# Kernel optimization log

Hardware: AMD Instinct MI355X
Metric: run time of the kernel (lower is better)

The kernel has to match this reference:

```python
import jax, jax.numpy as jnp
import numpy as np

SEQ, B, I, H = 2048, 64, 512, 512


def setup_inputs() -> dict:
    key = jax.random.key(0)
    ks = jax.random.split(key, 5)
    s = 1.0 / np.sqrt(H)  # torch.nn.RNN init scale
    return {
        "x": jax.random.normal(ks[0], (SEQ, B, I), dtype=jnp.float32),
        "W_ih": jax.random.normal(ks[1], (H, I), dtype=jnp.float32) * s,
        "W_hh": jax.random.normal(ks[2], (H, H), dtype=jnp.float32) * s,
        "b_ih": jax.random.normal(ks[3], (H,), dtype=jnp.float32) * s,
        "b_hh": jax.random.normal(ks[4], (H,), dtype=jnp.float32) * s,
    }


def reference(x, W_ih, W_hh, b_ih, b_hh):
    # Precompute input projection for all timesteps in one big GEMM: [T,B,H]
    xw = jnp.einsum("tbi,hi->tbh", x, W_ih) + b_ih + b_hh

    def step(h, xt):
        # h: [B,H]; xt: [B,H] (already includes x_t W_ih^T + biases)
        h = jnp.tanh(xt + h @ W_hh.T)
        return h, h

    h0 = jnp.zeros((x.shape[1], W_hh.shape[0]), dtype=x.dtype)
    _, out = jax.lax.scan(step, h0, xw)  # out: [T,B,H]
    return out.reshape(-1, W_hh.shape[0])  # [T*B, H], matches out.view(-1, hidden)
```

## Files before the change

### kernel.cpp

```cpp
#include <hip/hip_runtime.h>
#include <cmath>


#define SEQ_T 2048
#define BATCH 64
#define KDIM 512
#define HDIM 512

typedef __fp16 h2v __attribute__((ext_vector_type(2)));
typedef __fp16 f16x8 __attribute__((ext_vector_type(8)));
typedef float f32x4 __attribute__((ext_vector_type(4)));

static __device__ __forceinline__ f16x8 pk8(float4 a, float4 b) {
  h2v p0 = __builtin_amdgcn_cvt_pkrtz(a.x, a.y);
  h2v p1 = __builtin_amdgcn_cvt_pkrtz(a.z, a.w);
  h2v p2 = __builtin_amdgcn_cvt_pkrtz(b.x, b.y);
  h2v p3 = __builtin_amdgcn_cvt_pkrtz(b.z, b.w);
  f16x8 r;
  r[0] = p0[0]; r[1] = p0[1]; r[2] = p1[0]; r[3] = p1[1];
  r[4] = p2[0]; r[5] = p2[1]; r[6] = p3[0]; r[7] = p3[1];
  return r;
}


#define G_LDA 72

#define MFM(mt, nt) \
  d##mt##nt = __builtin_amdgcn_mfma_f32_16x16x32_f16(fa##mt, fb##nt, d##mt##nt, 0, 0, 0);

#define EPI(mt, nt, bb)                                                     \
  {                                                                         \
    int row = m0 + wm + mt * 16 + (l >> 4) * 4;                             \
    int col = n0 + wn + nt * 16 + (l & 15);                                 \
    out[(size_t)(row + 0) * HDIM + col] = d##mt##nt[0] + bb;                \
    out[(size_t)(row + 1) * HDIM + col] = d##mt##nt[1] + bb;                \
    out[(size_t)(row + 2) * HDIM + col] = d##mt##nt[2] + bb;                \
    out[(size_t)(row + 3) * HDIM + col] = d##mt##nt[3] + bb;                \
  }

__global__ __launch_bounds__(256) void xw_gemm(const float* __restrict__ x,
                                               const float* __restrict__ Wih,
                                               const float* __restrict__ bih,
                                               const float* __restrict__ bhh,
                                               float* __restrict__ out) {
  __shared__ __fp16 At[128 * G_LDA];
  __shared__ __fp16 Bt[64 * G_LDA];
  const int tid = threadIdx.x;
  const int l = tid & 63;
  const int w = tid >> 6;
  const int m0 = (blockIdx.x >> 3) * 128;
  const int n0 = (blockIdx.x & 7) * 64;
  const int wm = (w >> 1) * 64;
  const int wn = (w & 1) * 32;

  const float bias0 = bih[n0 + wn + (l & 15)] + bhh[n0 + wn + (l & 15)];
  const float bias1 = bih[n0 + wn + 16 + (l & 15)] + bhh[n0 + wn + 16 + (l & 15)];

  f32x4 d00 = {0,0,0,0}, d01 = {0,0,0,0}, d10 = {0,0,0,0}, d11 = {0,0,0,0};
  f32x4 d20 = {0,0,0,0}, d21 = {0,0,0,0}, d30 = {0,0,0,0}, d31 = {0,0,0,0};

  for (int k0 = 0; k0 < KDIM; k0 += 64) {
    __syncthreads();
#pragma unroll
    for (int p = 0; p < 4; ++p) {
      int idx = tid + p * 256;
      int r = idx >> 3, sg = idx & 7;
      const float* ps = x + (size_t)(m0 + r) * KDIM + k0 + sg * 8;
      *(f16x8*)(At + r * G_LDA + sg * 8) =
          pk8(*(const float4*)ps, *(const float4*)(ps + 4));
    }
#pragma unroll
    for (int p = 0; p < 2; ++p) {
      int idx = tid + p * 256;
      int r = idx >> 3, sg = idx & 7;
      const float* ps = Wih + (size_t)(n0 + r) * KDIM + k0 + sg * 8;
      *(f16x8*)(Bt + r * G_LDA + sg * 8) =
          pk8(*(const float4*)ps, *(const float4*)(ps + 4));
    }
    __syncthreads();
#pragma unroll
    for (int kk = 0; kk < 2; ++kk) {
      const int kc = kk * 32 + (l >> 4) * 8;
      f16x8 fa0 = *(const f16x8*)(At + (wm + 0 * 16 + (l & 15)) * G_LDA + kc);
      f16x8 fa1 = *(const f16x8*)(At + (wm + 1 * 16 + (l & 15)) * G_LDA + kc);
      f16x8 fa2 = *(const f16x8*)(At + (wm + 2 * 16 + (l & 15)) * G_LDA + kc);
      f16x8 fa3 = *(const f16x8*)(At + (wm + 3 * 16 + (l & 15)) * G_LDA + kc);
      f16x8 fb0 = *(const f16x8*)(Bt + (wn + 0 * 16 + (l & 15)) * G_LDA + kc);
      f16x8 fb1 = *(const f16x8*)(Bt + (wn + 1 * 16 + (l & 15)) * G_LDA + kc);
      MFM(0, 0) MFM(1, 0) MFM(2, 0) MFM(3, 0)
      MFM(0, 1) MFM(1, 1) MFM(2, 1) MFM(3, 1)
    }
  }

  EPI(0, 0, bias0) EPI(1, 0, bias0) EPI(2, 0, bias0) EPI(3, 0, bias0)
  EPI(0, 1, bias1) EPI(1, 1, bias1) EPI(2, 1, bias1) EPI(3, 1, bias1)
}


#define REPB(M, c) M(c,0) M(c,1) M(c,2) M(c,3) M(c,4) M(c,5) \
                   M(c,6) M(c,7) M(c,8) M(c,9) M(c,10) M(c,11)

#define DECLB(c, n) f16x8 bf##c##_##n;
#define LOADB(c, n)                                        \
  {                                                        \
    const float* p = wr##c + 32 * n;                       \
    bf##c##_##n = pk8(*(const float4*)p, *(const float4*)(p + 4)); \
  }
#define STOREB(c, n)                                                        \
  {                                                                         \
    const float* p = wr##c + 32 * n;                                        \
    *(f16x8*)(ldsm + ((n - 12) * 4 + c) * 8192 + (tid << 4)) =              \
        pk8(*(const float4*)p, *(const float4*)(p + 4));                    \
  }

#define MF(c, n) \
  d##c = __builtin_amdgcn_mfma_f32_16x16x32_f16(acur, bf##c##_##n, d##c, 0, 0, 0);
#define MFL(c, n)                                                           \
  {                                                                         \
    f16x8 bl = *(const f16x8*)(ldsm + ((n - 12) * 4 + c) * 8192 + (tid << 4)); \
    d##c = __builtin_amdgcn_mfma_f32_16x16x32_f16(acur, bl, d##c, 0, 0, 0); \
  }

#define CH(n, nn)                                                \
  {                                                              \
    f16x8 anx = *(const f16x8*)(hcv + 64 * (nn) + goff);         \
    MF(0, n) MF(1, n) MF(2, n) MF(3, n)                          \
    acur = anx;                                                  \
  }
#define CHL(n, nn)                                               \
  {                                                              \
    f16x8 anx = *(const f16x8*)(hcv + 64 * (nn) + goff);         \
    MFL(0, n) MFL(1, n) MFL(2, n) MFL(3, n)                      \
    acur = anx;                                                  \
  }

#define WLDS_BYTES (16 * 8192)
#define HBUF0 WLDS_BYTES
#define LDS_TOTAL (WLDS_BYTES + 3 * 1024)

__global__ __attribute__((amdgpu_flat_work_group_size(512, 512),
                          amdgpu_waves_per_eu(2, 2)))
void rnn_scan(const float* __restrict__ Whh, float* __restrict__ io) {
  extern __shared__ __align__(16) char ldsm[];
  const int tid = threadIdx.x;
  const int b = blockIdx.x;
  const int l = tid & 63;
  const int w = tid >> 6;
  const int m16 = l & 15;
  const int gh = l >> 4;
  const int goff = gh << 4;
  const int rb = w << 6;
  const int jo = rb + l;

  const float* wr0 = Whh + (size_t)(rb + 0 + m16) * KDIM + 8 * gh;
  const float* wr1 = Whh + (size_t)(rb + 16 + m16) * KDIM + 8 * gh;
  const float* wr2 = Whh + (size_t)(rb + 32 + m16) * KDIM + 8 * gh;
  const float* wr3 = Whh + (size_t)(rb + 48 + m16) * KDIM + 8 * gh;

  REPB(DECLB, 0) REPB(DECLB, 1) REPB(DECLB, 2) REPB(DECLB, 3)
  REPB(LOADB, 0) REPB(LOADB, 1) REPB(LOADB, 2) REPB(LOADB, 3)

  STOREB(0, 12) STOREB(1, 12) STOREB(2, 12) STOREB(3, 12)
  STOREB(0, 13) STOREB(1, 13) STOREB(2, 13) STOREB(3, 13)
  STOREB(0, 14) STOREB(1, 14) STOREB(2, 14) STOREB(3, 14)
  STOREB(0, 15) STOREB(1, 15) STOREB(2, 15) STOREB(3, 15)

  if (tid < 512) ((unsigned short*)(ldsm + HBUF0))[tid] = 0;
  __syncthreads();

  char* hcur = ldsm + HBUF0;
  char* hnxt = ldsm + HBUF0 + 1024;
  char* hthr = ldsm + HBUF0 + 2048;

  float* iorow = io + (size_t)b * HDIM;

  for (int t = 0; t < SEQ_T; ++t) {
    float uin = iorow[jo];

    const char* hcv = hcur;
    f16x8 acur = *(const f16x8*)(hcv + goff);

    f32x4 d0 = {0.f, 0.f, 0.f, 0.f};
    f32x4 d1 = {0.f, 0.f, 0.f, 0.f};
    f32x4 d2 = {0.f, 0.f, 0.f, 0.f};
    f32x4 d3 = {0.f, 0.f, 0.f, 0.f};

    CH(0, 1)  CH(1, 2)  CH(2, 3)   CH(3, 4)   CH(4, 5)   CH(5, 6)
    CH(6, 7)  CH(7, 8)  CH(8, 9)   CH(9, 10)  CH(10, 11) CH(11, 12)
    CHL(12, 13) CHL(13, 14) CHL(14, 15) CHL(15, 15)

    float za = (l & 16) ? d1[0] : d0[0];
    float zb = (l & 16) ? d3[0] : d2[0];
    float zs = (l & 32) ? zb : za;

    float z = uin + zs;
    float e = __expf(2.0f * z);
    float hn = 1.0f - 2.0f * __builtin_amdgcn_rcpf(e + 1.0f);
    iorow[jo] = hn;
    *(__fp16*)(hnxt + 2 * jo) = (__fp16)hn;

    char* tmp = hcur;
    hcur = hnxt; hnxt = hthr; hthr = tmp;
    iorow += (size_t)BATCH * HDIM;
    __syncthreads();
  }
}

extern "C" void kernel_launch(void* const* d_in, const int* in_sizes, int n_in,
                              void* d_out, int out_size, void* d_ws, size_t ws_size,
                              hipStream_t stream) {
  const float* x = (const float*)d_in[0];
  const float* Wih = (const float*)d_in[1];
  const float* Whh = (const float*)d_in[2];
  const float* bih = (const float*)d_in[3];
  const float* bhh = (const float*)d_in[4];
  float* out = (float*)d_out;

  (void)hipFuncSetAttribute((const void*)rnn_scan,
                            hipFuncAttributeMaxDynamicSharedMemorySize,
                            LDS_TOTAL);

  const int M = SEQ_T * BATCH;
  dim3 g1((M / 128) * (HDIM / 64));
  xw_gemm<<<g1, 256, 0, stream>>>(x, Wih, bih, bhh, out);

  rnn_scan<<<BATCH, 512, LDS_TOTAL, stream>>>(Whh, out);
}
```

Baseline: 3.358 ms.

## Stream half of W_hh fragments from global per step instead of LDS

A new prep kernel packs the upper half of W_hh (k-chunks 8-15) into fp16 MFMA fragment layout in the workspace. The scan kernel keeps only chunks 0-7 in registers and reloads the other half from global memory (L2-resident) every timestep, interleaved with the MFMAs. LDS use drops to the 3 KB hidden-state buffers. This removes the per-step LDS reads of weights and frees registers, but adds global/L2 load latency on the serial critical path of every step.

```diff
diff --git a/kernel.cpp b/kernel.cpp
--- a/kernel.cpp
+++ b/kernel.cpp
@@ -22,6 +22,15 @@
   return r;
 }
 
+__global__ __launch_bounds__(256) void w_prep(const float* __restrict__ Whh,
+                                              f16x8* __restrict__ ws) {
+  int v = blockIdx.x * 256 + threadIdx.x;
+  int l = v & 63, w = (v >> 6) & 7, c = (v >> 9) & 3, n = (v >> 11) + 8;
+  int row = 64 * w + 16 * c + (l & 15);
+  int col = 32 * n + 8 * (l >> 4);
+  const float* p = Whh + (size_t)row * KDIM + col;
+  ws[v] = pk8(*(const float4*)p, *(const float4*)(p + 4));
+}
 
 #define G_LDA 72
 
@@ -97,8 +106,7 @@
 }
 
 
-#define REPB(M, c) M(c,0) M(c,1) M(c,2) M(c,3) M(c,4) M(c,5) \
-                   M(c,6) M(c,7) M(c,8) M(c,9) M(c,10) M(c,11)
+#define REPB(M, c) M(c,0) M(c,1) M(c,2) M(c,3) M(c,4) M(c,5) M(c,6) M(c,7)
 
 #define DECLB(c, n) f16x8 bf##c##_##n;
 #define LOADB(c, n)                                        \
@@ -106,20 +114,18 @@
     const float* p = wr##c + 32 * n;                       \
     bf##c##_##n = pk8(*(const float4*)p, *(const float4*)(p + 4)); \
   }
-#define STOREB(c, n)                                                        \
-  {                                                                         \
-    const float* p = wr##c + 32 * n;                                        \
-    *(f16x8*)(ldsm + ((n - 12) * 4 + c) * 8192 + (tid << 4)) =              \
-        pk8(*(const float4*)p, *(const float4*)(p + 4));                    \
-  }
+
+#define DECLS(n) f16x8 sv0_##n, sv1_##n, sv2_##n, sv3_##n;
+#define LOADS(n)                                  \
+  sv0_##n = wsp[((n - 8) * 4 + 0) * 512];         \
+  sv1_##n = wsp[((n - 8) * 4 + 1) * 512];         \
+  sv2_##n = wsp[((n - 8) * 4 + 2) * 512];         \
+  sv3_##n = wsp[((n - 8) * 4 + 3) * 512];
 
 #define MF(c, n) \
   d##c = __builtin_amdgcn_mfma_f32_16x16x32_f16(acur, bf##c##_##n, d##c, 0, 0, 0);
-#define MFL(c, n)                                                           \
-  {                                                                         \
-    f16x8 bl = *(const f16x8*)(ldsm + ((n - 12) * 4 + c) * 8192 + (tid << 4)); \
-    d##c = __builtin_amdgcn_mfma_f32_16x16x32_f16(acur, bl, d##c, 0, 0, 0); \
-  }
+#define MS(c, n) \
+  d##c = __builtin_amdgcn_mfma_f32_16x16x32_f16(acur, sv##c##_##n, d##c, 0, 0, 0);
 
 #define CH(n, nn)                                                \
   {                                                              \
@@ -127,21 +133,18 @@
     MF(0, n) MF(1, n) MF(2, n) MF(3, n)                          \
     acur = anx;                                                  \
   }
-#define CHL(n, nn)                                               \
+#define CST(n, nn)                                               \
   {                                                              \
     f16x8 anx = *(const f16x8*)(hcv + 64 * (nn) + goff);         \
-    MFL(0, n) MFL(1, n) MFL(2, n) MFL(3, n)                      \
+    MS(0, n) MS(1, n) MS(2, n) MS(3, n)                          \
     acur = anx;                                                  \
   }
-
-#define WLDS_BYTES (16 * 8192)
-#define HBUF0 WLDS_BYTES
-#define LDS_TOTAL (WLDS_BYTES + 3 * 1024)
 
 __global__ __attribute__((amdgpu_flat_work_group_size(512, 512),
                           amdgpu_waves_per_eu(2, 2)))
-void rnn_scan(const float* __restrict__ Whh, float* __restrict__ io) {
-  extern __shared__ __align__(16) char ldsm[];
+void rnn_scan(const float* __restrict__ Whh, const f16x8* __restrict__ ws,
+              float* __restrict__ io) {
+  __shared__ __align__(16) char ldsm[3 * 1024];
   const int tid = threadIdx.x;
   const int b = blockIdx.x;
   const int l = tid & 63;
@@ -160,19 +163,19 @@
   REPB(DECLB, 0) REPB(DECLB, 1) REPB(DECLB, 2) REPB(DECLB, 3)
   REPB(LOADB, 0) REPB(LOADB, 1) REPB(LOADB, 2) REPB(LOADB, 3)
 
-  STOREB(0, 12) STOREB(1, 12) STOREB(2, 12) STOREB(3, 12)
-  STOREB(0, 13) STOREB(1, 13) STOREB(2, 13) STOREB(3, 13)
-  STOREB(0, 14) STOREB(1, 14) STOREB(2, 14) STOREB(3, 14)
-  STOREB(0, 15) STOREB(1, 15) STOREB(2, 15) STOREB(3, 15)
-
-  if (tid < 512) ((unsigned short*)(ldsm + HBUF0))[tid] = 0;
+  const f16x8* wsp = ws + (w * 64 + l);
+
+  if (tid < 512) ((unsigned short*)ldsm)[tid] = 0;
   __syncthreads();
 
-  char* hcur = ldsm + HBUF0;
-  char* hnxt = ldsm + HBUF0 + 1024;
-  char* hthr = ldsm + HBUF0 + 2048;
+  char* hcur = ldsm;
+  char* hnxt = ldsm + 1024;
+  char* hthr = ldsm + 2048;
 
   float* iorow = io + (size_t)b * HDIM;
+
+  DECLS(8) DECLS(9) DECLS(10) DECLS(11)
+  DECLS(12) DECLS(13) DECLS(14) DECLS(15)
 
   for (int t = 0; t < SEQ_T; ++t) {
     float uin = iorow[jo];
@@ -185,9 +188,17 @@
     f32x4 d2 = {0.f, 0.f, 0.f, 0.f};
     f32x4 d3 = {0.f, 0.f, 0.f, 0.f};
 
-    CH(0, 1)  CH(1, 2)  CH(2, 3)   CH(3, 4)   CH(4, 5)   CH(5, 6)
-    CH(6, 7)  CH(7, 8)  CH(8, 9)   CH(9, 10)  CH(10, 11) CH(11, 12)
-    CHL(12, 13) CHL(13, 14) CHL(14, 15) CHL(15, 15)
+    LOADS(8) LOADS(9)
+    CH(0, 1) CH(1, 2) CH(2, 3)
+    LOADS(10) LOADS(11)
+    CH(3, 4) CH(4, 5) CH(5, 6)
+    LOADS(12) LOADS(13)
+    CH(6, 7) CH(7, 8)
+    CST(8, 9) CST(9, 10)
+    LOADS(14) LOADS(15)
+    CST(10, 11) CST(11, 12)
+    CST(12, 13) CST(13, 14)
+    CST(14, 15) CST(15, 15)
 
     float za = (l & 16) ? d1[0] : d0[0];
     float zb = (l & 16) ? d3[0] : d2[0];
@@ -215,14 +226,13 @@
   const float* bih = (const float*)d_in[3];
   const float* bhh = (const float*)d_in[4];
   float* out = (float*)d_out;
-
-  (void)hipFuncSetAttribute((const void*)rnn_scan,
-                            hipFuncAttributeMaxDynamicSharedMemorySize,
-                            LDS_TOTAL);
+  f16x8* ws = (f16x8*)d_ws;
+
+  w_prep<<<64, 256, 0, stream>>>(Whh, ws);
 
   const int M = SEQ_T * BATCH;
   dim3 g1((M / 128) * (HDIM / 64));
   xw_gemm<<<g1, 256, 0, stream>>>(x, Wih, bih, bhh, out);
 
-  rnn_scan<<<BATCH, 512, LDS_TOTAL, stream>>>(Whh, out);
-}
+  rnn_scan<<<BATCH, 512, 0, stream>>>(Whh, ws, out);
+}
```

Result: slower. 5.746 ms (+71.1%).

## Stream last W_hh chunks from global fp16 workspace each step, shrink register-resident weights

Applied to the files above, without the earlier changes.

Cuts the register-resident W_hh fragments from 12 to 8 k-chunks per column group and moves chunks 8-11 into LDS. The last four chunks (12-15) are pre-converted to fp16 by a new w_prep kernel into the workspace and reloaded from global/L2 on every timestep. The intent is to relieve register pressure, and the per-step global reloads are expected to hit in cache. The per-step barrier is also replaced with an explicit lgkmcnt wait plus s_barrier. The cost is a global-load latency on the serial recurrence critical path at every step.

```diff
diff --git a/kernel.cpp b/kernel.cpp
--- a/kernel.cpp
+++ b/kernel.cpp
@@ -22,6 +22,15 @@
   return r;
 }
 
+__global__ __launch_bounds__(256) void w_prep(const float* __restrict__ Whh,
+                                              f16x8* __restrict__ ws) {
+  int v = blockIdx.x * 256 + threadIdx.x;
+  int l = v & 63, w = (v >> 6) & 7, c = (v >> 9) & 3, n = (v >> 11) + 12;
+  int row = 64 * w + 16 * c + (l & 15);
+  int col = 32 * n + 8 * (l >> 4);
+  const float* p = Whh + (size_t)row * KDIM + col;
+  ws[v] = pk8(*(const float4*)p, *(const float4*)(p + 4));
+}
 
 #define G_LDA 72
 
@@ -97,8 +106,7 @@
 }
 
 
-#define REPB(M, c) M(c,0) M(c,1) M(c,2) M(c,3) M(c,4) M(c,5) \
-                   M(c,6) M(c,7) M(c,8) M(c,9) M(c,10) M(c,11)
+#define REPB(M, c) M(c,0) M(c,1) M(c,2) M(c,3) M(c,4) M(c,5) M(c,6) M(c,7)
 
 #define DECLB(c, n) f16x8 bf##c##_##n;
 #define LOADB(c, n)                                        \
@@ -109,17 +117,26 @@
 #define STOREB(c, n)                                                        \
   {                                                                         \
     const float* p = wr##c + 32 * n;                                        \
-    *(f16x8*)(ldsm + ((n - 12) * 4 + c) * 8192 + (tid << 4)) =              \
+    *(f16x8*)(ldsm + (((n) - 8) * 4 + c) * 8192 + (tid << 4)) =             \
         pk8(*(const float4*)p, *(const float4*)(p + 4));                    \
   }
+
+#define DECLS(n) f16x8 sv0_##n, sv1_##n, sv2_##n, sv3_##n;
+#define LOADS(n)                                   \
+  sv0_##n = wsp[((n - 12) * 4 + 0) * 512];         \
+  sv1_##n = wsp[((n - 12) * 4 + 1) * 512];         \
+  sv2_##n = wsp[((n - 12) * 4 + 2) * 512];         \
+  sv3_##n = wsp[((n - 12) * 4 + 3) * 512];
 
 #define MF(c, n) \
   d##c = __builtin_amdgcn_mfma_f32_16x16x32_f16(acur, bf##c##_##n, d##c, 0, 0, 0);
-#define MFL(c, n)                                                           \
-  {                                                                         \
-    f16x8 bl = *(const f16x8*)(ldsm + ((n - 12) * 4 + c) * 8192 + (tid << 4)); \
-    d##c = __builtin_amdgcn_mfma_f32_16x16x32_f16(acur, bl, d##c, 0, 0, 0); \
-  }
+#define MFL(c, n)                                                              \
+  {                                                                            \
+    f16x8 bl = *(const f16x8*)(ldsm + (((n) - 8) * 4 + c) * 8192 + (tid << 4)); \
+    d##c = __builtin_amdgcn_mfma_f32_16x16x32_f16(acur, bl, d##c, 0, 0, 0);    \
+  }
+#define MS(c, n) \
+  d##c = __builtin_amdgcn_mfma_f32_16x16x32_f16(acur, sv##c##_##n, d##c, 0, 0, 0);
 
 #define CH(n, nn)                                                \
   {                                                              \
@@ -133,14 +150,27 @@
     MFL(0, n) MFL(1, n) MFL(2, n) MFL(3, n)                      \
     acur = anx;                                                  \
   }
+#define CST(n, nn)                                               \
+  {                                                              \
+    f16x8 anx = *(const f16x8*)(hcv + 64 * (nn) + goff);         \
+    MS(0, n) MS(1, n) MS(2, n) MS(3, n)                          \
+    acur = anx;                                                  \
+  }
 
 #define WLDS_BYTES (16 * 8192)
 #define HBUF0 WLDS_BYTES
 #define LDS_TOTAL (WLDS_BYTES + 3 * 1024)
 
+#define BAR()                                              \
+  asm volatile("s_waitcnt lgkmcnt(0)" ::: "memory");       \
+  __builtin_amdgcn_sched_barrier(0);                       \
+  __builtin_amdgcn_s_barrier();                            \
+  __builtin_amdgcn_sched_barrier(0);
+
 __global__ __attribute__((amdgpu_flat_work_group_size(512, 512),
                           amdgpu_waves_per_eu(2, 2)))
-void rnn_scan(const float* __restrict__ Whh, float* __restrict__ io) {
+void rnn_scan(const float* __restrict__ Whh, const f16x8* __restrict__ ws,
+              float* __restrict__ io) {
   extern __shared__ __align__(16) char ldsm[];
   const int tid = threadIdx.x;
   const int b = blockIdx.x;
@@ -160,10 +190,12 @@
   REPB(DECLB, 0) REPB(DECLB, 1) REPB(DECLB, 2) REPB(DECLB, 3)
   REPB(LOADB, 0) REPB(LOADB, 1) REPB(LOADB, 2) REPB(LOADB, 3)
 
-  STOREB(0, 12) STOREB(1, 12) STOREB(2, 12) STOREB(3, 12)
-  STOREB(0, 13) STOREB(1, 13) STOREB(2, 13) STOREB(3, 13)
-  STOREB(0, 14) STOREB(1, 14) STOREB(2, 14) STOREB(3, 14)
-  STOREB(0, 15) STOREB(1, 15) STOREB(2, 15) STOREB(3, 15)
+  STOREB(0, 8)  STOREB(1, 8)  STOREB(2, 8)  STOREB(3, 8)
+  STOREB(0, 9)  STOREB(1, 9)  STOREB(2, 9)  STOREB(3, 9)
+  STOREB(0, 10) STOREB(1, 10) STOREB(2, 10) STOREB(3, 10)
+  STOREB(0, 11) STOREB(1, 11) STOREB(2, 11) STOREB(3, 11)
+
+  const f16x8* wsp = ws + (w * 64 + l);
 
   if (tid < 512) ((unsigned short*)(ldsm + HBUF0))[tid] = 0;
   __syncthreads();
@@ -174,8 +206,12 @@
 
   float* iorow = io + (size_t)b * HDIM;
 
+  DECLS(12) DECLS(13) DECLS(14) DECLS(15)
+
   for (int t = 0; t < SEQ_T; ++t) {
     float uin = iorow[jo];
+
+    LOADS(12) LOADS(13) LOADS(14) LOADS(15)
 
     const char* hcv = hcur;
     f16x8 acur = *(const f16x8*)(hcv + goff);
@@ -185,9 +221,10 @@
     f32x4 d2 = {0.f, 0.f, 0.f, 0.f};
     f32x4 d3 = {0.f, 0.f, 0.f, 0.f};
 
-    CH(0, 1)  CH(1, 2)  CH(2, 3)   CH(3, 4)   CH(4, 5)   CH(5, 6)
-    CH(6, 7)  CH(7, 8)  CH(8, 9)   CH(9, 10)  CH(10, 11) CH(11, 12)
-    CHL(12, 13) CHL(13, 14) CHL(14, 15) CHL(15, 15)
+    CH(0, 1)  CH(1, 2)   CH(2, 3)   CH(3, 4)
+    CH(4, 5)  CH(5, 6)   CH(6, 7)   CH(7, 8)
+    CHL(8, 9) CHL(9, 10) CHL(10, 11) CHL(11, 12)
+    CST(12, 13) CST(13, 14) CST(14, 15) CST(15, 15)
 
     float za = (l & 16) ? d1[0] : d0[0];
     float zb = (l & 16) ? d3[0] : d2[0];
@@ -202,7 +239,7 @@
     char* tmp = hcur;
     hcur = hnxt; hnxt = hthr; hthr = tmp;
     iorow += (size_t)BATCH * HDIM;
-    __syncthreads();
+    BAR();
   }
 }
 
@@ -215,14 +252,17 @@
   const float* bih = (const float*)d_in[3];
   const float* bhh = (const float*)d_in[4];
   float* out = (float*)d_out;
+  f16x8* ws = (f16x8*)d_ws;
 
   (void)hipFuncSetAttribute((const void*)rnn_scan,
                             hipFuncAttributeMaxDynamicSharedMemorySize,
                             LDS_TOTAL);
 
+  w_prep<<<32, 256, 0, stream>>>(Whh, ws);
+
   const int M = SEQ_T * BATCH;
   dim3 g1((M / 128) * (HDIM / 64));
   xw_gemm<<<g1, 256, 0, stream>>>(x, Wih, bih, bhh, out);
 
-  rnn_scan<<<BATCH, 512, LDS_TOTAL, stream>>>(Whh, out);
-}
+  rnn_scan<<<BATCH, 512, LDS_TOTAL, stream>>>(Whh, ws, out);
+}
```

Measured after the change: 3.526 ms. +5.0%, slower.

## Halve scan workgroup to 4 waves, each computing 128 hidden units

Applied to the files above, without the earlier changes.

The recurrent scan kernel now uses 256 threads (4 waves) per batch row instead of 512. Each wave owns 128 output rows with 8 MFMA accumulators, and its register-resident slice of W_hh grows to 96 f16x8 fragments. The per-step __syncthreads is replaced by a manual lgkmcnt wait plus s_barrier. The aim is cheaper barriers and more MFMA work per wave on the latency-bound serial loop, at the cost of heavy register pressure (waves_per_eu 1) and less parallelism per step.

```diff
diff --git a/kernel.cpp b/kernel.cpp
--- a/kernel.cpp
+++ b/kernel.cpp
@@ -21,7 +21,6 @@
   r[4] = p2[0]; r[5] = p2[1]; r[6] = p3[0]; r[7] = p3[1];
   return r;
 }
-
 
 #define G_LDA 72
 
@@ -97,49 +96,56 @@
 }
 
 
-#define REPB(M, c) M(c,0) M(c,1) M(c,2) M(c,3) M(c,4) M(c,5) \
-                   M(c,6) M(c,7) M(c,8) M(c,9) M(c,10) M(c,11)
+#define REPC(M, n) M(0,n) M(1,n) M(2,n) M(3,n) M(4,n) M(5,n) M(6,n) M(7,n)
 
 #define DECLB(c, n) f16x8 bf##c##_##n;
-#define LOADB(c, n)                                        \
-  {                                                        \
-    const float* p = wr##c + 32 * n;                       \
-    bf##c##_##n = pk8(*(const float4*)p, *(const float4*)(p + 4)); \
-  }
-#define STOREB(c, n)                                                        \
-  {                                                                         \
-    const float* p = wr##c + 32 * n;                                        \
-    *(f16x8*)(ldsm + ((n - 12) * 4 + c) * 8192 + (tid << 4)) =              \
-        pk8(*(const float4*)p, *(const float4*)(p + 4));                    \
+#define LOADB(c, n)                                                  \
+  {                                                                  \
+    const float* p = wr##c + 32 * n;                                 \
+    bf##c##_##n = pk8(*(const float4*)p, *(const float4*)(p + 4));   \
+  }
+#define STOREB(c, n)                                                 \
+  {                                                                  \
+    const float* p = wr##c + 32 * n;                                 \
+    *(f16x8*)(ldsm + (((n) - 12) * 8 + c) * 4096 + (tid << 4)) =     \
+        pk8(*(const float4*)p, *(const float4*)(p + 4));             \
   }
 
 #define MF(c, n) \
   d##c = __builtin_amdgcn_mfma_f32_16x16x32_f16(acur, bf##c##_##n, d##c, 0, 0, 0);
-#define MFL(c, n)                                                           \
-  {                                                                         \
-    f16x8 bl = *(const f16x8*)(ldsm + ((n - 12) * 4 + c) * 8192 + (tid << 4)); \
-    d##c = __builtin_amdgcn_mfma_f32_16x16x32_f16(acur, bl, d##c, 0, 0, 0); \
+#define MFL(c, n)                                                               \
+  {                                                                             \
+    f16x8 bl = *(const f16x8*)(ldsm + (((n) - 12) * 8 + c) * 4096 + (tid << 4)); \
+    d##c = __builtin_amdgcn_mfma_f32_16x16x32_f16(acur, bl, d##c, 0, 0, 0);     \
   }
 
 #define CH(n, nn)                                                \
   {                                                              \
     f16x8 anx = *(const f16x8*)(hcv + 64 * (nn) + goff);         \
     MF(0, n) MF(1, n) MF(2, n) MF(3, n)                          \
+    MF(4, n) MF(5, n) MF(6, n) MF(7, n)                          \
     acur = anx;                                                  \
   }
 #define CHL(n, nn)                                               \
   {                                                              \
     f16x8 anx = *(const f16x8*)(hcv + 64 * (nn) + goff);         \
     MFL(0, n) MFL(1, n) MFL(2, n) MFL(3, n)                      \
+    MFL(4, n) MFL(5, n) MFL(6, n) MFL(7, n)                      \
     acur = anx;                                                  \
   }
 
-#define WLDS_BYTES (16 * 8192)
+#define WLDS_BYTES (32 * 4096)
 #define HBUF0 WLDS_BYTES
 #define LDS_TOTAL (WLDS_BYTES + 3 * 1024)
 
-__global__ __attribute__((amdgpu_flat_work_group_size(512, 512),
-                          amdgpu_waves_per_eu(2, 2)))
+#define BAR()                                              \
+  asm volatile("s_waitcnt lgkmcnt(0)" ::: "memory");       \
+  __builtin_amdgcn_sched_barrier(0);                       \
+  __builtin_amdgcn_s_barrier();                            \
+  __builtin_amdgcn_sched_barrier(0);
+
+__global__ __attribute__((amdgpu_flat_work_group_size(256, 256),
+                          amdgpu_waves_per_eu(1, 1)))
 void rnn_scan(const float* __restrict__ Whh, float* __restrict__ io) {
   extern __shared__ __align__(16) char ldsm[];
   const int tid = threadIdx.x;
@@ -149,23 +155,30 @@
   const int m16 = l & 15;
   const int gh = l >> 4;
   const int goff = gh << 4;
-  const int rb = w << 6;
-  const int jo = rb + l;
-
-  const float* wr0 = Whh + (size_t)(rb + 0 + m16) * KDIM + 8 * gh;
-  const float* wr1 = Whh + (size_t)(rb + 16 + m16) * KDIM + 8 * gh;
-  const float* wr2 = Whh + (size_t)(rb + 32 + m16) * KDIM + 8 * gh;
-  const float* wr3 = Whh + (size_t)(rb + 48 + m16) * KDIM + 8 * gh;
-
-  REPB(DECLB, 0) REPB(DECLB, 1) REPB(DECLB, 2) REPB(DECLB, 3)
-  REPB(LOADB, 0) REPB(LOADB, 1) REPB(LOADB, 2) REPB(LOADB, 3)
-
-  STOREB(0, 12) STOREB(1, 12) STOREB(2, 12) STOREB(3, 12)
-  STOREB(0, 13) STOREB(1, 13) STOREB(2, 13) STOREB(3, 13)
-  STOREB(0, 14) STOREB(1, 14) STOREB(2, 14) STOREB(3, 14)
-  STOREB(0, 15) STOREB(1, 15) STOREB(2, 15) STOREB(3, 15)
-
-  if (tid < 512) ((unsigned short*)(ldsm + HBUF0))[tid] = 0;
+  const int rb = w << 7;
+  const int jo0 = rb + l;
+  const int jo1 = rb + 64 + l;
+
+  const float* wr0 = Whh + (size_t)(rb + 0   + m16) * KDIM + 8 * gh;
+  const float* wr1 = Whh + (size_t)(rb + 16  + m16) * KDIM + 8 * gh;
+  const float* wr2 = Whh + (size_t)(rb + 32  + m16) * KDIM + 8 * gh;
+  const float* wr3 = Whh + (size_t)(rb + 48  + m16) * KDIM + 8 * gh;
+  const float* wr4 = Whh + (size_t)(rb + 64  + m16) * KDIM + 8 * gh;
+  const float* wr5 = Whh + (size_t)(rb + 80  + m16) * KDIM + 8 * gh;
+  const float* wr6 = Whh + (size_t)(rb + 96  + m16) * KDIM + 8 * gh;
+  const float* wr7 = Whh + (size_t)(rb + 112 + m16) * KDIM + 8 * gh;
+
+  REPC(DECLB, 0)  REPC(DECLB, 1)  REPC(DECLB, 2)  REPC(DECLB, 3)
+  REPC(DECLB, 4)  REPC(DECLB, 5)  REPC(DECLB, 6)  REPC(DECLB, 7)
+  REPC(DECLB, 8)  REPC(DECLB, 9)  REPC(DECLB, 10) REPC(DECLB, 11)
+  REPC(LOADB, 0)  REPC(LOADB, 1)  REPC(LOADB, 2)  REPC(LOADB, 3)
+  REPC(LOADB, 4)  REPC(LOADB, 5)  REPC(LOADB, 6)  REPC(LOADB, 7)
+  REPC(LOADB, 8)  REPC(LOADB, 9)  REPC(LOADB, 10) REPC(LOADB, 11)
+
+  REPC(STOREB, 12) REPC(STOREB, 13) REPC(STOREB, 14) REPC(STOREB, 15)
+
+  ((unsigned short*)(ldsm + HBUF0))[tid] = 0;
+  ((unsigned short*)(ldsm + HBUF0))[tid + 256] = 0;
   __syncthreads();
 
   char* hcur = ldsm + HBUF0;
@@ -175,34 +188,44 @@
   float* iorow = io + (size_t)b * HDIM;
 
   for (int t = 0; t < SEQ_T; ++t) {
-    float uin = iorow[jo];
+    float uin0 = iorow[jo0];
+    float uin1 = iorow[jo1];
 
     const char* hcv = hcur;
     f16x8 acur = *(const f16x8*)(hcv + goff);
 
-    f32x4 d0 = {0.f, 0.f, 0.f, 0.f};
-    f32x4 d1 = {0.f, 0.f, 0.f, 0.f};
-    f32x4 d2 = {0.f, 0.f, 0.f, 0.f};
-    f32x4 d3 = {0.f, 0.f, 0.f, 0.f};
-
-    CH(0, 1)  CH(1, 2)  CH(2, 3)   CH(3, 4)   CH(4, 5)   CH(5, 6)
-    CH(6, 7)  CH(7, 8)  CH(8, 9)   CH(9, 10)  CH(10, 11) CH(11, 12)
+    f32x4 d0 = {0.f,0.f,0.f,0.f}, d1 = {0.f,0.f,0.f,0.f};
+    f32x4 d2 = {0.f,0.f,0.f,0.f}, d3 = {0.f,0.f,0.f,0.f};
+    f32x4 d4 = {0.f,0.f,0.f,0.f}, d5 = {0.f,0.f,0.f,0.f};
+    f32x4 d6 = {0.f,0.f,0.f,0.f}, d7 = {0.f,0.f,0.f,0.f};
+
+    CH(0, 1)   CH(1, 2)   CH(2, 3)   CH(3, 4)
+    CH(4, 5)   CH(5, 6)   CH(6, 7)   CH(7, 8)
+    CH(8, 9)   CH(9, 10)  CH(10, 11) CH(11, 12)
     CHL(12, 13) CHL(13, 14) CHL(14, 15) CHL(15, 15)
 
-    float za = (l & 16) ? d1[0] : d0[0];
-    float zb = (l & 16) ? d3[0] : d2[0];
-    float zs = (l & 32) ? zb : za;
-
-    float z = uin + zs;
-    float e = __expf(2.0f * z);
-    float hn = 1.0f - 2.0f * __builtin_amdgcn_rcpf(e + 1.0f);
-    iorow[jo] = hn;
-    *(__fp16*)(hnxt + 2 * jo) = (__fp16)hn;
+    float za0 = (l & 16) ? d1[0] : d0[0];
+    float zb0 = (l & 16) ? d3[0] : d2[0];
+    float z0s = (l & 32) ? zb0 : za0;
+    float za1 = (l & 16) ? d5[0] : d4[0];
+    float zb1 = (l & 16) ? d7[0] : d6[0];
+    float z1s = (l & 32) ? zb1 : za1;
+
+    float z0 = uin0 + z0s;
+    float z1 = uin1 + z1s;
+    float e0 = __expf(2.0f * z0);
+    float e1 = __expf(2.0f * z1);
+    float h0 = 1.0f - 2.0f * __builtin_amdgcn_rcpf(e0 + 1.0f);
+    float h1 = 1.0f - 2.0f * __builtin_amdgcn_rcpf(e1 + 1.0f);
+    iorow[jo0] = h0;
+    iorow[jo1] = h1;
+    *(__fp16*)(hnxt + 2 * jo0) = (__fp16)h0;
+    *(__fp16*)(hnxt + 2 * jo1) = (__fp16)h1;
 
     char* tmp = hcur;
     hcur = hnxt; hnxt = hthr; hthr = tmp;
     iorow += (size_t)BATCH * HDIM;
-    __syncthreads();
+    BAR();
   }
 }
 
@@ -224,5 +247,5 @@
   dim3 g1((M / 128) * (HDIM / 64));
   xw_gemm<<<g1, 256, 0, stream>>>(x, Wih, bih, bhh, out);
 
-  rnn_scan<<<BATCH, 512, LDS_TOTAL, stream>>>(Whh, out);
-}
+  rnn_scan<<<BATCH, 256, LDS_TOTAL, stream>>>(Whh, out);
+}
```

After: 6.336 ms. 1.89x slower.
